# Optimization experiments

Hardware: AMD Instinct MI355X
Metric: run time of the kernel (lower is better)

Reference implementation:

```python
import jax, jax.numpy as jnp
import numpy as np

B, T, C, H = 8, 2048, 1024, 128  # batch, seq, embed_dim, head_size

def setup_inputs() -> dict:
    key = jax.random.key(0)
    kx, kk, kq, kv = jax.random.split(key, 4)
    s = 1.0 / np.sqrt(C)  # ~nn.Linear init scale
    return {
        "x": jax.random.normal(kx, (B, T, C), dtype=jnp.float32),
        "Wk": jax.random.normal(kk, (H, C), dtype=jnp.float32) * s,
        "Wq": jax.random.normal(kq, (H, C), dtype=jnp.float32) * s,
        "Wv": jax.random.normal(kv, (H, C), dtype=jnp.float32) * s,
    }

def reference(x, Wk, Wq, Wv):
    b, t, c = x.shape
    # Faithful to source: q uses the KEY projection (bug in original); Wq is unused.
    k = jnp.einsum('btc,hc->bth', x, Wk)   # [B,T,H]
    q = jnp.einsum('btc,hc->bth', x, Wk)   # [B,T,H]  (self.key used for q)
    v = jnp.einsum('btc,hc->bth', x, Wv)   # [B,T,H]
    score = jnp.einsum('bqh,bkh->bqk', q, k) * (c ** -0.5)  # scale by C, per source
    causal = jnp.tril(jnp.ones((t, t), dtype=bool))
    score = jnp.where(causal, score, -jnp.inf)
    attn = jax.nn.softmax(score, axis=-1)   # [B,T,T]
    out = jnp.einsum('bqk,bkh->bqh', attn, v)  # [B,T,H]
    return out
```

## Files before the change

### kernel.cpp

```cpp
#include <hip/hip_runtime.h>
#include <hip/hip_bf16.h>

#define BATCH 8
#define SEQ   2048
#define EMB   1024
#define HD    128

typedef __attribute__((ext_vector_type(8))) short bf16x8;
typedef __attribute__((ext_vector_type(4))) float f32x4;

__device__ __forceinline__ short f2bf(float f) {
    union { float f; unsigned u; } v; v.f = f;
    unsigned r = v.u + 0x7fffu + ((v.u >> 16) & 1u);
    return (short)(r >> 16);
}


__global__ void prep_w(const float* __restrict__ Wk, const float* __restrict__ Wv,
                       short* __restrict__ Wimg) {
    int g  = blockIdx.x * 256 + threadIdx.x;
    int q  = g & 3;
    int l  = (g >> 2) & 15;
    int f  = (g >> 6) & 7;
    int kk = (g >> 9) & 1;
    int kc = (g >> 10) & 15;
    int nh = (g >> 14) & 1;
    const float* src = (nh ? Wv : Wk) + (size_t)(f * 16 + l) * EMB + kc * 64 + kk * 32 + q * 8;
    float4 f0 = *(const float4*)src;
    float4 f1 = *(const float4*)(src + 4);
    bf16x8 v;
    v[0]=f2bf(f0.x); v[1]=f2bf(f0.y); v[2]=f2bf(f0.z); v[3]=f2bf(f0.w);
    v[4]=f2bf(f1.x); v[5]=f2bf(f1.y); v[6]=f2bf(f1.z); v[7]=f2bf(f1.w);
    *(bf16x8*)&Wimg[(size_t)g * 8] = v;
}

__global__ __launch_bounds__(512, 2)
void proj_kernel(const float* __restrict__ x, const short* __restrict__ Wimg,
                 short* __restrict__ Kimg,
                 short* __restrict__ Vimg)
{
    __shared__ __align__(16) union {
        short A[2][64][72];
        short ep[16384];
    } sm;

    const int tid  = threadIdx.x;
    const int wave = tid >> 6;
    const int lane = tid & 63;
    const int quad = lane >> 4;
    const int l16  = lane & 15;
    const int nh   = wave >> 2;
    const int fb   = (wave & 3) * 2;
    const int mt   = blockIdx.x;
    const int row0 = mt * 64;

    const int srow = tid >> 3, sseg = tid & 7;
    const float* xsrc = x + (size_t)(row0 + srow) * EMB + sseg * 8;
    const short* wsrc = Wimg + (size_t)nh * 131072;

    f32x4 acc[4][2];
#pragma unroll
    for (int a = 0; a < 4; ++a)
#pragma unroll
        for (int c = 0; c < 2; ++c) acc[a][c] = f32x4{0.f, 0.f, 0.f, 0.f};

    {
        float4 a0 = *(const float4*)xsrc;
        float4 a1 = *(const float4*)(xsrc + 4);
        bf16x8 v;
        v[0]=f2bf(a0.x); v[1]=f2bf(a0.y); v[2]=f2bf(a0.z); v[3]=f2bf(a0.w);
        v[4]=f2bf(a1.x); v[5]=f2bf(a1.y); v[6]=f2bf(a1.z); v[7]=f2bf(a1.w);
        *(bf16x8*)&sm.A[0][srow][sseg * 8] = v;
    }
    __syncthreads();

    for (int kc = 0; kc < 16; ++kc) {
        const int cur = kc & 1;
        float4 a0, a1;
        if (kc < 15) {
            const float* nx = xsrc + (kc + 1) * 64;
            a0 = *(const float4*)nx;
            a1 = *(const float4*)(nx + 4);
        }
        const short* wc = wsrc + (size_t)kc * 8192;
        bf16x8 bfr[2][2];
#pragma unroll
        for (int kk = 0; kk < 2; ++kk)
#pragma unroll
            for (int f2 = 0; f2 < 2; ++f2)
                bfr[kk][f2] = *(const bf16x8*)&wc[(((kk * 8 + fb + f2) * 16 + l16) * 4 + quad) * 8];

#pragma unroll
        for (int kk = 0; kk < 2; ++kk)
#pragma unroll
            for (int mf = 0; mf < 4; ++mf) {
                bf16x8 af = *(const bf16x8*)&sm.A[cur][mf * 16 + l16][kk * 32 + quad * 8];
#pragma unroll
                for (int f2 = 0; f2 < 2; ++f2)
                    acc[mf][f2] = __builtin_amdgcn_mfma_f32_16x16x32_bf16(af, bfr[kk][f2], acc[mf][f2], 0, 0, 0);
            }

        if (kc < 15) {
            bf16x8 v;
            v[0]=f2bf(a0.x); v[1]=f2bf(a0.y); v[2]=f2bf(a0.z); v[3]=f2bf(a0.w);
            v[4]=f2bf(a1.x); v[5]=f2bf(a1.y); v[6]=f2bf(a1.z); v[7]=f2bf(a1.w);
            *(bf16x8*)&sm.A[cur ^ 1][srow][sseg * 8] = v;
        }
        __syncthreads();
    }

#pragma unroll
    for (int mf = 0; mf < 4; ++mf)
#pragma unroll
        for (int f2 = 0; f2 < 2; ++f2)
#pragma unroll
            for (int r = 0; r < 4; ++r) {
                const int row = mf * 16 + quad * 4 + r;
                const int h   = (fb + f2) * 16 + l16;
                int idx;
                if (nh == 0)
                    idx = ((((h >> 5) * 4 + (row >> 4)) * 16 + (row & 15)) * 4 + ((h >> 3) & 3)) * 8 + (h & 7);
                else
                    idx = 8192 + ((((row >> 5) * 8 + (h >> 4)) * 16 + (h & 15)) * 4 + ((row >> 3) & 3)) * 8 + (row & 7);
                sm.ep[idx] = f2bf(acc[mf][f2][r]);
            }
    __syncthreads();

    {
#pragma unroll
        for (int i = 0; i < 4; ++i) {
            const int g = i * 512 + tid;
            short* dst = (g < 1024) ? (Kimg + (size_t)mt * 8192 + g * 8)
                                    : (Vimg + (size_t)mt * 8192 + (g - 1024) * 8);
            *(bf16x8*)dst = *(const bf16x8*)&sm.ep[g * 8];
        }
    }
}

#define LOG2E 1.4426950408889634f

__global__ __launch_bounds__(256, 2)
void attn_kernel(const short* __restrict__ Kimg,
                 const short* __restrict__ Vimg,
                 float* __restrict__ out)
{
    __shared__ __align__(16) short ps[4][1024];
    __shared__ float obuf[2][16][132];
    __shared__ float lbuf[2][16];

    const int tid  = threadIdx.x;
    const int wave = tid >> 6;
    const int lane = tid & 63;
    const int quad = lane >> 4;
    const int l16  = lane & 15;

    const int b    = blockIdx.x & 7;
    const int g    = blockIdx.x >> 3;
    const int pair = wave >> 1;
    const int p    = wave & 1;
    const int qt   = pair ? (127 - g) : g;
    const int n    = (qt >> 2) + 1;

    const short* Kb = Kimg + (size_t)b * 32 * 8192;
    const short* Vb = Vimg + (size_t)b * 32 * 8192;

    bf16x8 qf[4];
    {
        const short* qi = Kb + (size_t)(qt >> 2) * 8192;
        const int jsq = qt & 3;
#pragma unroll
        for (int kc = 0; kc < 4; ++kc)
            qf[kc] = *(const bf16x8*)&qi[(((kc * 4 + jsq) * 16 + l16) * 4 + quad) * 8];
    }

    f32x4 O[8];
#pragma unroll
    for (int f = 0; f < 8; ++f) O[f] = f32x4{0.f, 0.f, 0.f, 0.f};
    float lp[4] = {0.f, 0.f, 0.f, 0.f};

    const float coef = LOG2E * 0.03125f;
    short* psw = ps[wave];

    for (int jt = p; jt < n; jt += 2) {
        const short* ki = Kb + (size_t)jt * 8192;
        const short* vi = Vb + (size_t)jt * 8192;

        bf16x8 kfr[16];
#pragma unroll
        for (int kc = 0; kc < 4; ++kc)
#pragma unroll
            for (int js = 0; js < 4; ++js)
                kfr[kc * 4 + js] = *(const bf16x8*)&ki[(((kc * 4 + js) * 16 + l16) * 4 + quad) * 8];

        f32x4 S[4];
#pragma unroll
        for (int js = 0; js < 4; ++js) S[js] = f32x4{0.f, 0.f, 0.f, 0.f};
#pragma unroll
        for (int kc = 0; kc < 4; ++kc)
#pragma unroll
            for (int js = 0; js < 4; ++js)
                S[js] = __builtin_amdgcn_mfma_f32_16x16x32_bf16(qf[kc], kfr[kc * 4 + js], S[js], 0, 0, 0);

        bf16x8 vfr[16];
#pragma unroll
        for (int jc = 0; jc < 2; ++jc)
#pragma unroll
            for (int f = 0; f < 8; ++f)
                vfr[jc * 8 + f] = *(const bf16x8*)&vi[(((jc * 8 + f) * 16 + l16) * 4 + quad) * 8];

        const bool diag = (jt == n - 1);
#pragma unroll
        for (int js = 0; js < 4; ++js) {
            const int jj = jt * 64 + js * 16 + l16;
            const int cb = js * 2 + (l16 >> 3);
            const int e  = l16 & 7;
#pragma unroll
            for (int r = 0; r < 4; ++r) {
                float vv = S[js][r] * coef;
                if (diag && (jj > qt * 16 + quad * 4 + r)) vv = -INFINITY;
                float pe = exp2f(vv);
                lp[r] += pe;
                const int i8 = quad * 4 + r;
                psw[(i8 * 8 + (cb ^ (i8 & 7))) * 8 + e] = f2bf(pe);
            }
        }

#pragma unroll
        for (int jc = 0; jc < 2; ++jc) {
            const int pblk = l16 * 8 + ((jc * 4 + quad) ^ (l16 & 7));
            bf16x8 pa = *(const bf16x8*)&psw[pblk * 8];
#pragma unroll
            for (int f = 0; f < 8; ++f)
                O[f] = __builtin_amdgcn_mfma_f32_16x16x32_bf16(pa, vfr[jc * 8 + f], O[f], 0, 0, 0);
        }
    }

#pragma unroll
    for (int r = 0; r < 4; ++r) {
        float s = lp[r];
        s += __shfl_xor(s, 1);
        s += __shfl_xor(s, 2);
        s += __shfl_xor(s, 4);
        s += __shfl_xor(s, 8);
        lp[r] = s;
    }

    if (p == 1) {
#pragma unroll
        for (int f = 0; f < 8; ++f)
#pragma unroll
            for (int r = 0; r < 4; ++r)
                obuf[pair][quad * 4 + r][f * 16 + l16] = O[f][r];
        if (l16 == 0) {
#pragma unroll
            for (int r = 0; r < 4; ++r) lbuf[pair][quad * 4 + r] = lp[r];
        }
    }
    __syncthreads();

    if (p == 0) {
#pragma unroll
        for (int r = 0; r < 4; ++r) {
            const int row16 = quad * 4 + r;
            const float L   = lp[r] + lbuf[pair][row16];
            const float inv = 1.f / L;
            const int row   = qt * 16 + row16;
            float* dst = out + (size_t)(b * SEQ + row) * HD + l16;
#pragma unroll
            for (int f = 0; f < 8; ++f)
                dst[f * 16] = (O[f][r] + obuf[pair][row16][f * 16 + l16]) * inv;
        }
    }
}

extern "C" void kernel_launch(void* const* d_in, const int* in_sizes, int n_in,
                              void* d_out, int out_size, void* d_ws, size_t ws_size,
                              hipStream_t stream) {
    const float* x  = (const float*)d_in[0];
    const float* Wk = (const float*)d_in[1];
    const float* Wv = (const float*)d_in[3];
    float* out = (float*)d_out;

    short* Wimg = (short*)d_ws;
    short* Kimg = Wimg + (size_t)262144;
    short* Vimg = Kimg + (size_t)BATCH * 32 * 8192;

    prep_w<<<128, 256, 0, stream>>>(Wk, Wv, Wimg);
    proj_kernel<<<256, 512, 0, stream>>>(x, Wimg, Kimg, Vimg);
    attn_kernel<<<512, 256, 0, stream>>>(Kimg, Vimg, out);
}
```

Measured before the change: 149.7 us.

## Stage K/V tiles in LDS with async double-buffered loads shared across waves

The attention kernel now assigns two adjacent 16-row query tiles per block, and each wave pair splits the key columns and output head dimension instead of splitting the KV loop. K and V tiles are copied into LDS with global_load_lds, and K is double-buffered so the next tile's load overlaps the current compute. This replaces redundant per-wave global fragment loads and removes the cross-wave O reduction through shared memory. In exchange it adds two barriers per iteration, uses more LDS, and drops the old pairing of light and heavy query tiles in favour of a new block ordering.

```diff
diff --git a/kernel.cpp b/kernel.cpp
--- a/kernel.cpp
+++ b/kernel.cpp
@@ -13,6 +13,12 @@
     union { float f; unsigned u; } v; v.f = f;
     unsigned r = v.u + 0x7fffu + ((v.u >> 16) & 1u);
     return (short)(r >> 16);
+}
+
+__device__ __forceinline__ void glds16(const short* g, short* l) {
+    __builtin_amdgcn_global_load_lds(
+        (const __attribute__((address_space(1))) unsigned int*)g,
+        (__attribute__((address_space(3))) unsigned int*)l, 16, 0, 0);
 }
 
 
@@ -144,9 +150,10 @@
                  const short* __restrict__ Vimg,
                  float* __restrict__ out)
 {
-    __shared__ __align__(16) short ps[4][1024];
-    __shared__ float obuf[2][16][132];
-    __shared__ float lbuf[2][16];
+    __shared__ __align__(16) short kbuf[2][8192];
+    __shared__ __align__(16) short vbuf[8192];
+    __shared__ __align__(16) short ps[2][1024];
+    __shared__ float lsum[4][16];
 
     const int tid  = threadIdx.x;
     const int wave = tid >> 6;
@@ -155,11 +162,12 @@
     const int l16  = lane & 15;
 
     const int b    = blockIdx.x & 7;
-    const int g    = blockIdx.x >> 3;
-    const int pair = wave >> 1;
+    const int gg   = blockIdx.x >> 3;
+    const int G    = (blockIdx.x < 256) ? (63 - gg) : (gg - 32);
+    const int qsel = wave >> 1;
     const int p    = wave & 1;
-    const int qt   = pair ? (127 - g) : g;
-    const int n    = (qt >> 2) + 1;
+    const int qt   = 2 * G + qsel;
+    const int n    = (G >> 1) + 1;
 
     const short* Kb = Kimg + (size_t)b * 32 * 8192;
     const short* Vb = Vimg + (size_t)b * 32 * 8192;
@@ -173,66 +181,85 @@
             qf[kc] = *(const bf16x8*)&qi[(((kc * 4 + jsq) * 16 + l16) * 4 + quad) * 8];
     }
 
-    f32x4 O[8];
-#pragma unroll
-    for (int f = 0; f < 8; ++f) O[f] = f32x4{0.f, 0.f, 0.f, 0.f};
+    f32x4 O[4];
+#pragma unroll
+    for (int f = 0; f < 4; ++f) O[f] = f32x4{0.f, 0.f, 0.f, 0.f};
     float lp[4] = {0.f, 0.f, 0.f, 0.f};
 
     const float coef = LOG2E * 0.03125f;
-    short* psw = ps[wave];
-
-    for (int jt = p; jt < n; jt += 2) {
-        const short* ki = Kb + (size_t)jt * 8192;
-        const short* vi = Vb + (size_t)jt * 8192;
-
-        bf16x8 kfr[16];
+    short* psq = ps[qsel];
+
+    {
+        const short* sk = Kb + wave * 2048 + lane * 8;
+#pragma unroll
+        for (int i = 0; i < 4; ++i)
+            glds16(sk + i * 512, &kbuf[0][wave * 2048 + i * 512]);
+    }
+
+    int cur = 0;
+    for (int jt = 0; jt < n; ++jt) {
+        asm volatile("s_waitcnt vmcnt(0)" ::: "memory");
+        __builtin_amdgcn_s_barrier();
+
+        {
+            const short* sv = Vb + (size_t)jt * 8192 + wave * 2048 + lane * 8;
+#pragma unroll
+            for (int i = 0; i < 4; ++i)
+                glds16(sv + i * 512, &vbuf[wave * 2048 + i * 512]);
+        }
+        const bool more = (jt + 1 < n);
+        if (more) {
+            const short* sk = Kb + (size_t)(jt + 1) * 8192 + wave * 2048 + lane * 8;
+#pragma unroll
+            for (int i = 0; i < 4; ++i)
+                glds16(sk + i * 512, &kbuf[cur ^ 1][wave * 2048 + i * 512]);
+        }
+
+        const short* kt = kbuf[cur];
+        f32x4 S[2];
+        S[0] = f32x4{0.f, 0.f, 0.f, 0.f};
+        S[1] = f32x4{0.f, 0.f, 0.f, 0.f};
 #pragma unroll
         for (int kc = 0; kc < 4; ++kc)
 #pragma unroll
-            for (int js = 0; js < 4; ++js)
-                kfr[kc * 4 + js] = *(const bf16x8*)&ki[(((kc * 4 + js) * 16 + l16) * 4 + quad) * 8];
-
-        f32x4 S[4];
-#pragma unroll
-        for (int js = 0; js < 4; ++js) S[js] = f32x4{0.f, 0.f, 0.f, 0.f};
-#pragma unroll
-        for (int kc = 0; kc < 4; ++kc)
-#pragma unroll
-            for (int js = 0; js < 4; ++js)
-                S[js] = __builtin_amdgcn_mfma_f32_16x16x32_bf16(qf[kc], kfr[kc * 4 + js], S[js], 0, 0, 0);
-
-        bf16x8 vfr[16];
-#pragma unroll
-        for (int jc = 0; jc < 2; ++jc)
-#pragma unroll
-            for (int f = 0; f < 8; ++f)
-                vfr[jc * 8 + f] = *(const bf16x8*)&vi[(((jc * 8 + f) * 16 + l16) * 4 + quad) * 8];
+            for (int j2 = 0; j2 < 2; ++j2) {
+                bf16x8 kf = *(const bf16x8*)&kt[((kc * 4 + p * 2 + j2) * 64 + l16 * 4 + quad) * 8];
+                S[j2] = __builtin_amdgcn_mfma_f32_16x16x32_bf16(qf[kc], kf, S[j2], 0, 0, 0);
+            }
 
         const bool diag = (jt == n - 1);
 #pragma unroll
-        for (int js = 0; js < 4; ++js) {
+        for (int j2 = 0; j2 < 2; ++j2) {
+            const int js = p * 2 + j2;
             const int jj = jt * 64 + js * 16 + l16;
             const int cb = js * 2 + (l16 >> 3);
             const int e  = l16 & 7;
 #pragma unroll
             for (int r = 0; r < 4; ++r) {
-                float vv = S[js][r] * coef;
+                float vv = S[j2][r] * coef;
                 if (diag && (jj > qt * 16 + quad * 4 + r)) vv = -INFINITY;
                 float pe = exp2f(vv);
                 lp[r] += pe;
                 const int i8 = quad * 4 + r;
-                psw[(i8 * 8 + (cb ^ (i8 & 7))) * 8 + e] = f2bf(pe);
-            }
-        }
+                psq[(i8 * 8 + (cb ^ (i8 & 7))) * 8 + e] = f2bf(pe);
+            }
+        }
+
+        if (more) asm volatile("s_waitcnt vmcnt(4) lgkmcnt(0)" ::: "memory");
+        else      asm volatile("s_waitcnt vmcnt(0) lgkmcnt(0)" ::: "memory");
+        __builtin_amdgcn_s_barrier();
 
 #pragma unroll
         for (int jc = 0; jc < 2; ++jc) {
             const int pblk = l16 * 8 + ((jc * 4 + quad) ^ (l16 & 7));
-            bf16x8 pa = *(const bf16x8*)&psw[pblk * 8];
-#pragma unroll
-            for (int f = 0; f < 8; ++f)
-                O[f] = __builtin_amdgcn_mfma_f32_16x16x32_bf16(pa, vfr[jc * 8 + f], O[f], 0, 0, 0);
-        }
+            bf16x8 pa = *(const bf16x8*)&psq[pblk * 8];
+#pragma unroll
+            for (int fo = 0; fo < 4; ++fo) {
+                bf16x8 vf = *(const bf16x8*)&vbuf[((jc * 8 + p * 4 + fo) * 64 + l16 * 4 + quad) * 8];
+                O[fo] = __builtin_amdgcn_mfma_f32_16x16x32_bf16(pa, vf, O[fo], 0, 0, 0);
+            }
+        }
+        cur ^= 1;
     }
 
 #pragma unroll
@@ -244,32 +271,22 @@
         s += __shfl_xor(s, 8);
         lp[r] = s;
     }
-
-    if (p == 1) {
-#pragma unroll
-        for (int f = 0; f < 8; ++f)
-#pragma unroll
-            for (int r = 0; r < 4; ++r)
-                obuf[pair][quad * 4 + r][f * 16 + l16] = O[f][r];
-        if (l16 == 0) {
-#pragma unroll
-            for (int r = 0; r < 4; ++r) lbuf[pair][quad * 4 + r] = lp[r];
-        }
+    if (l16 == 0) {
+#pragma unroll
+        for (int r = 0; r < 4; ++r) lsum[wave][quad * 4 + r] = lp[r];
     }
     __syncthreads();
 
-    if (p == 0) {
-#pragma unroll
-        for (int r = 0; r < 4; ++r) {
-            const int row16 = quad * 4 + r;
-            const float L   = lp[r] + lbuf[pair][row16];
-            const float inv = 1.f / L;
-            const int row   = qt * 16 + row16;
-            float* dst = out + (size_t)(b * SEQ + row) * HD + l16;
-#pragma unroll
-            for (int f = 0; f < 8; ++f)
-                dst[f * 16] = (O[f][r] + obuf[pair][row16][f * 16 + l16]) * inv;
-        }
+#pragma unroll
+    for (int r = 0; r < 4; ++r) {
+        const int row16 = quad * 4 + r;
+        const float L   = lsum[qsel * 2][row16] + lsum[qsel * 2 + 1][row16];
+        const float inv = 1.f / L;
+        const int row   = qt * 16 + row16;
+        float* dst = out + (size_t)(b * SEQ + row) * HD + p * 64 + l16;
+#pragma unroll
+        for (int fo = 0; fo < 4; ++fo)
+            dst[fo * 16] = O[fo][r] * inv;
     }
 }
 
```

Measured after the change: 143.8 us. 1.04x faster.
